# Kernel tuning notes

Hardware: AMD Instinct MI355X
Metric: run time of the kernel (lower is better)

The kernel has to match this reference:

```python
import jax, jax.numpy as jnp
import numpy as np

N_NODES = 100000
N_EDGES = 1280000
N_REL = 8
DIM = 64
N_LAYERS = 2
N_TGT = 50000


def setup_inputs() -> dict:
    key = jax.random.key(0)
    ks = jax.random.split(key, 8)
    x_idx = jnp.arange(N_NODES, dtype=jnp.int64) if jax.config.jax_enable_x64 else jnp.arange(N_NODES, dtype=jnp.int32)
    edge_index = jax.random.randint(ks[0], (2, N_EDGES), 0, N_NODES)
    edge_type = jax.random.randint(ks[1], (N_EDGES,), 0, N_REL)
    target_edge_index = jax.random.randint(ks[2], (2, N_TGT), 0, N_NODES)
    # xavier-ish scales to keep activations stable through relu stack
    node_emb = jax.random.normal(ks[3], (N_NODES, DIM), dtype=jnp.float32) * 0.1
    weight = jax.random.normal(ks[4], (N_LAYERS, N_REL, DIM, DIM), dtype=jnp.float32) * (1.0 / np.sqrt(DIM))
    root = jax.random.normal(ks[5], (N_LAYERS, DIM, DIM), dtype=jnp.float32) * (1.0 / np.sqrt(DIM))
    bias = jax.random.normal(ks[6], (N_LAYERS, DIM), dtype=jnp.float32) * 0.01
    return {"x_idx": x_idx, "edge_index": edge_index, "edge_type": edge_type,
            "target_edge_index": target_edge_index, "node_emb": node_emb,
            "weight": weight, "root": root, "bias": bias}


def reference(x_idx, edge_index, edge_type, target_edge_index, node_emb, weight, root, bias):
    # RGCN forward: x = node_emb[x_idx]; L x (FastRGCNConv + relu); edge dot-product score.
    x = node_emb[x_idx]                       # [N, D]
    src, dst = edge_index[0], edge_index[1]   # messages flow src -> dst (PyG source_to_target)
    n = x.shape[0]
    # in-degree for 'mean' aggregation (zero-degree nodes get 0, guard div)
    deg = jax.ops.segment_sum(jnp.ones((src.shape[0],), dtype=x.dtype), dst, num_segments=n)
    inv_deg = (1.0 / jnp.maximum(deg, 1.0))[:, None]  # [N, 1]
    n_layers = weight.shape[0]
    for l in range(n_layers):
        # transform every node by every relation, then gather per edge (FastRGCNConv math)
        h = jnp.einsum('ni,rio->rno', x, weight[l])   # [R, N, D]
        msg = h[edge_type, src]                       # [E, D]
        agg = jax.ops.segment_sum(msg, dst, num_segments=n) * inv_deg  # mean aggr [N, D]
        x = jax.nn.relu(agg + x @ root[l] + bias[l])
    s, t = target_edge_index[0], target_edge_index[1]
    return jnp.sum(x[s] * x[t], axis=-1)              # [T]
```

## Files before the change

kernel.cpp:

```cpp
#include <hip/hip_runtime.h>
#include <hip/hip_bf16.h>

#define DIM 64
#define NREL 8
#define KTOT 576

typedef __bf16 bf16x8 __attribute__((ext_vector_type(8)));
typedef __bf16 bf16x4 __attribute__((ext_vector_type(4)));
typedef float  f32x4  __attribute__((ext_vector_type(4)));

__global__ __launch_bounds__(256) void histgather_kernel(const int* __restrict__ dst,
                                                         const int* __restrict__ et,
                                                         int* __restrict__ deg8,
                                                         int* __restrict__ eoff,
                                                         const int* __restrict__ x_idx,
                                                         const float* __restrict__ emb,
                                                         __bf16* __restrict__ xb0,
                                                         __bf16* __restrict__ hbuf,
                                                         int* __restrict__ srcs,
                                                         int N, int E, int epad_cap) {
    int i = blockIdx.x * 256 + threadIdx.x;
    if (i < N * DIM) {
        int n = i >> 6;
        int c = i & 63;
        xb0[i] = (__bf16)emb[(size_t)x_idx[n] * DIM + c];
    }
    if (i < DIM) {
        hbuf[(size_t)N * NREL * DIM + i] = (__bf16)0.f;
    }
    if (i < epad_cap) srcs[i] = N * NREL;
    if (i < E) eoff[i] = atomicAdd(&deg8[dst[i] * 8 + et[i]], 1);
}

__global__ __launch_bounds__(256) void scan1rp_kernel(const int* __restrict__ deg8,
                                                      int* __restrict__ gtotal,
                                                      float* __restrict__ invdeg,
                                                      int* __restrict__ rp,
                                                      int* __restrict__ rend,
                                                      const float* __restrict__ weight,
                                                      const float* __restrict__ root,
                                                      __bf16* __restrict__ Wt2,
                                                      int N, int L) {
    __shared__ int sd[256];
    __shared__ int sbase;
    int tid = threadIdx.x;
    int d = blockIdx.x * 256 + tid;
    int dv[NREL];
    int vpad = 0;
    if (d < N) {
        int vtrue = 0;
#pragma unroll
        for (int r = 0; r < NREL; ++r) { dv[r] = deg8[d * 8 + r]; vtrue += dv[r]; }
        vpad = (vtrue + 3) & ~3;
        invdeg[d] = 1.0f / fmaxf((float)vtrue, 1.0f);
    }
    sd[tid] = vpad;
    __syncthreads();
#pragma unroll
    for (int off = 1; off < 256; off <<= 1) {
        int t = (tid >= off) ? sd[tid - off] : 0;
        __syncthreads();
        sd[tid] += t;
        __syncthreads();
    }
    if (tid == 255) sbase = atomicAdd(gtotal, sd[255]);
    __syncthreads();
    if (d < N) {
        int base = sbase + sd[tid] - vpad;
        int run = 0;
#pragma unroll
        for (int r = 0; r < NREL; ++r) {
            rp[d * 8 + r] = base + run;
            run += dv[r];
        }
        rend[d] = base + vpad;
    }
    int total = L * KTOT * DIM;
    for (int idx = blockIdx.x * 256 + tid; idx < total; idx += gridDim.x * 256) {
        int l = idx / (KTOT * DIM);
        int rem = idx - l * (KTOT * DIM);
        int row = rem / DIM;
        int ch = rem - row * DIM;
        float w;
        if (row < 512) {
            int r = row >> 6, c = row & 63;
            w = weight[(((l * 8 + r) * 64) + ch) * 64 + c];
        } else {
            w = root[(l * 64 + ch) * 64 + (row - 512)];
        }
        Wt2[idx] = (__bf16)w;
    }
}

__global__ __launch_bounds__(256) void bucket_kernel(const int* __restrict__ src,
                                                     const int* __restrict__ dst,
                                                     const int* __restrict__ et,
                                                     const int* __restrict__ rp,
                                                     const int* __restrict__ eoff,
                                                     int* __restrict__ srcs, int E) {
    int i = blockIdx.x * 256 + threadIdx.x;
    int half = (E + 1) >> 1;
    if (i >= half) return;
    int iB = i + half;
    bool hasB = iB < E;
    int etA = et[i];
    int etB = hasB ? et[iB] : 0;
    int cellA = dst[i] * 8 + etA;
    int cellB = hasB ? dst[iB] * 8 + etB : 0;
    int rA = rp[cellA];
    int rB = hasB ? rp[cellB] : 0;
    int oA = eoff[i];
    int oB = hasB ? eoff[iB] : 0;
    int sA = src[i];
    int sB = hasB ? src[iB] : 0;
    srcs[rA + oA] = sA * NREL + etA;
    if (hasB) srcs[rB + oB] = sB * NREL + etB;
}

__global__ __launch_bounds__(256) void transform_kernel(const __bf16* __restrict__ xin,
                                                        const __bf16* __restrict__ Wt2,
                                                        __bf16* __restrict__ h, int N) {
    int wave = threadIdx.x >> 6;
    int lane = threadIdx.x & 63;
    int l15 = lane & 15;
    int lg  = lane >> 4;

    bf16x8 afrag[8][2];
#pragma unroll
    for (int p = 0; p < 8; ++p) {
        const __bf16* wrow = Wt2 + (size_t)(p * 64 + 16 * wave + l15) * DIM + lg * 8;
        afrag[p][0] = *reinterpret_cast<const bf16x8*>(wrow);
        afrag[p][1] = *reinterpret_cast<const bf16x8*>(wrow + 32);
    }
    int cb = 16 * wave + 4 * lg;

    int ntiles = (N + 15) >> 4;
    for (int tile = blockIdx.x; tile < ntiles; tile += gridDim.x) {
        int n = tile * 16 + l15;
        int nc = (n < N) ? n : (N - 1);
        const __bf16* xrow = xin + (size_t)nc * DIM + lg * 8;
        bf16x8 bv0 = *reinterpret_cast<const bf16x8*>(xrow);
        bf16x8 bv1 = *reinterpret_cast<const bf16x8*>(xrow + 32);

#pragma unroll
        for (int p = 0; p < 8; ++p) {
            f32x4 acc = (f32x4){0.f, 0.f, 0.f, 0.f};
            acc = __builtin_amdgcn_mfma_f32_16x16x32_bf16(afrag[p][0], bv0, acc, 0, 0, 0);
            acc = __builtin_amdgcn_mfma_f32_16x16x32_bf16(afrag[p][1], bv1, acc, 0, 0, 0);
            if (n < N) {
                bf16x4 hv;
#pragma unroll
                for (int i = 0; i < 4; ++i) hv[i] = (__bf16)acc[i];
                *reinterpret_cast<bf16x4*>(h + (size_t)n * (NREL * DIM) + p * 64 + cb) = hv;
            }
        }
    }
}

__global__ __launch_bounds__(256) void aggroot_kernel(const __bf16* __restrict__ h,
                                                      const __bf16* __restrict__ xin,
                                                      const int* __restrict__ srcs,
                                                      const int* __restrict__ rp,
                                                      const int* __restrict__ rend,
                                                      const float* __restrict__ invdeg,
                                                      const __bf16* __restrict__ Wt2,
                                                      const float* __restrict__ bias_l,
                                                      __bf16* __restrict__ xout, int N) {
    __shared__ __align__(16) float S16[16][68];
    int wave = threadIdx.x >> 6;
    int lane = threadIdx.x & 63;
    int l15 = lane & 15;
    int lg  = lane >> 4;
    const int SENT = N * NREL;

    bf16x8 ar0, ar1;
    {
        const __bf16* wrow = Wt2 + (size_t)(512 + 16 * wave + l15) * DIM + lg * 8;
        ar0 = *reinterpret_cast<const bf16x8*>(wrow);
        ar1 = *reinterpret_cast<const bf16x8*>(wrow + 32);
    }
    int cbase = 16 * wave + 4 * lg;
    f32x4 bias4 = *reinterpret_cast<const f32x4*>(bias_l + cbase);

    int tile = blockIdx.x;

#pragma unroll
    for (int rr = 0; rr < 4; ++rr) {
        int d0 = tile * 16 + wave * 4 + rr;
        if (d0 >= N) d0 = N - 1;
        int d = __builtin_amdgcn_readfirstlane(d0);
        int qb = rp[d * 8];
        int qe = rend[d];
        float acc = 0.f;
        for (int q = qb; q < qe; q += 16) {
            int rem = qe - q;
            int4 sa = *reinterpret_cast<const int4*>(srcs + q);
            int4 sb = *reinterpret_cast<const int4*>(srcs + q + 4);
            int4 sc = *reinterpret_cast<const int4*>(srcs + q + 8);
            int4 sd = *reinterpret_cast<const int4*>(srcs + q + 12);
            bool vb = rem >= 8, vc = rem >= 12, vd = rem >= 16;
            int i0 = sa.x,              i1 = sa.y,              i2 = sa.z,              i3 = sa.w;
            int i4 = vb ? sb.x : SENT,  i5 = vb ? sb.y : SENT,  i6 = vb ? sb.z : SENT,  i7 = vb ? sb.w : SENT;
            int i8 = vc ? sc.x : SENT,  i9 = vc ? sc.y : SENT,  iA = vc ? sc.z : SENT,  iB = vc ? sc.w : SENT;
            int iC = vd ? sd.x : SENT,  iD = vd ? sd.y : SENT,  iE = vd ? sd.z : SENT,  iF = vd ? sd.w : SENT;
            float v0 = (float)h[(size_t)i0 * DIM + lane];
            float v1 = (float)h[(size_t)i1 * DIM + lane];
            float v2 = (float)h[(size_t)i2 * DIM + lane];
            float v3 = (float)h[(size_t)i3 * DIM + lane];
            float v4 = (float)h[(size_t)i4 * DIM + lane];
            float v5 = (float)h[(size_t)i5 * DIM + lane];
            float v6 = (float)h[(size_t)i6 * DIM + lane];
            float v7 = (float)h[(size_t)i7 * DIM + lane];
            float v8 = (float)h[(size_t)i8 * DIM + lane];
            float v9 = (float)h[(size_t)i9 * DIM + lane];
            float vA = (float)h[(size_t)iA * DIM + lane];
            float vB = (float)h[(size_t)iB * DIM + lane];
            float vC = (float)h[(size_t)iC * DIM + lane];
            float vD = (float)h[(size_t)iD * DIM + lane];
            float vE = (float)h[(size_t)iE * DIM + lane];
            float vF = (float)h[(size_t)iF * DIM + lane];
            acc += (((v0 + v1) + (v2 + v3)) + ((v4 + v5) + (v6 + v7)))
                 + (((v8 + v9) + (vA + vB)) + ((vC + vD) + (vE + vF)));
        }
        S16[wave * 4 + rr][lane] = acc * invdeg[d];
    }
    __syncthreads();

    int n = tile * 16 + l15;
    int nc = (n < N) ? n : (N - 1);
    const __bf16* xrow = xin + (size_t)nc * DIM + lg * 8;
    bf16x8 bv0 = *reinterpret_cast<const bf16x8*>(xrow);
    bf16x8 bv1 = *reinterpret_cast<const bf16x8*>(xrow + 32);
    f32x4 acc = (f32x4){0.f, 0.f, 0.f, 0.f};
    acc = __builtin_amdgcn_mfma_f32_16x16x32_bf16(ar0, bv0, acc, 0, 0, 0);
    acc = __builtin_amdgcn_mfma_f32_16x16x32_bf16(ar1, bv1, acc, 0, 0, 0);

    if (n < N) {
        f32x4 ag = *reinterpret_cast<const f32x4*>(&S16[l15][cbase]);
        bf16x4 hv;
#pragma unroll
        for (int i = 0; i < 4; ++i)
            hv[i] = (__bf16)fmaxf(acc[i] + ag[i] + bias4[i], 0.f);
        *reinterpret_cast<bf16x4*>(xout + (size_t)n * DIM + cbase) = hv;
    }
}

__global__ __launch_bounds__(256) void score_kernel(const __bf16* __restrict__ xb,
                                                    const int* __restrict__ s,
                                                    const int* __restrict__ t,
                                                    float* __restrict__ out, int T) {
    int i = blockIdx.x * 4 + (threadIdx.x >> 6);
    if (i >= T) return;
    int lane = threadIdx.x & 63;
    float p = (float)xb[(size_t)s[i] * DIM + lane] * (float)xb[(size_t)t[i] * DIM + lane];
#pragma unroll
    for (int off = 32; off > 0; off >>= 1) p += __shfl_down(p, off, 64);
    if (lane == 0) out[i] = p;
}

extern "C" void kernel_launch(void* const* d_in, const int* in_sizes, int n_in,
                              void* d_out, int out_size, void* d_ws, size_t ws_size,
                              hipStream_t stream) {
    const int*   x_idx  = (const int*)d_in[0];
    const int*   eidx   = (const int*)d_in[1];
    const int*   etyp   = (const int*)d_in[2];
    const int*   tidx   = (const int*)d_in[3];
    const float* emb    = (const float*)d_in[4];
    const float* weight = (const float*)d_in[5];
    const float* root   = (const float*)d_in[6];
    const float* bias   = (const float*)d_in[7];

    int N = in_sizes[0];
    int E = in_sizes[2];
    int T = in_sizes[3] / 2;
    int L = in_sizes[5] / (NREL * DIM * DIM);

    const int* src = eidx;
    const int* dst = eidx + E;
    const int* ts  = tidx;
    const int* tt  = tidx + T;
    float* out = (float*)d_out;

    int epad_cap = E + 3 * N + 64;

    char* p = (char*)d_ws;
    auto alloc = [&](size_t bytes) -> void* {
        void* r = (void*)p;
        p += (bytes + 255) & ~(size_t)255;
        return r;
    };
    __bf16* hbuf    = (__bf16*)alloc(((size_t)N * NREL + 1) * DIM * sizeof(__bf16));
    __bf16* xb0     = (__bf16*)alloc((size_t)N * DIM * sizeof(__bf16));
    __bf16* xb1     = (__bf16*)alloc((size_t)N * DIM * sizeof(__bf16));
    __bf16* Wt2     = (__bf16*)alloc((size_t)L * KTOT * DIM * sizeof(__bf16));
    int*    srcs    = (int*)   alloc((size_t)epad_cap * sizeof(int));
    int*    eoff    = (int*)   alloc((size_t)E * sizeof(int));
    int*    deg8    = (int*)   alloc(((size_t)N * 8 + 8) * sizeof(int));
    int*    rp      = (int*)   alloc((size_t)N * 8 * sizeof(int));
    int*    rend    = (int*)   alloc((size_t)N * sizeof(int));
    float*  invdeg  = (float*) alloc((size_t)N * sizeof(float));

    int* gtotal = deg8 + (size_t)N * 8;

    int nb = (N + 255) / 256;
    int ntiles = (N + 15) / 16;

    hipMemsetAsync(deg8, 0, ((size_t)N * 8 + 8) * sizeof(int), stream);
    histgather_kernel<<<((size_t)N * DIM + 255) / 256, 256, 0, stream>>>(
        dst, etyp, deg8, eoff, x_idx, emb, xb0, hbuf, srcs, N, E, epad_cap);
    scan1rp_kernel<<<nb, 256, 0, stream>>>(deg8, gtotal, invdeg, rp, rend,
                                           weight, root, Wt2, N, L);
    {
        int half = (E + 1) / 2;
        bucket_kernel<<<(half + 255) / 256, 256, 0, stream>>>(src, dst, etyp, rp, eoff, srcs, E);
    }

    __bf16* xcur = xb0;
    __bf16* xnxt = xb1;
    for (int l = 0; l < L; ++l) {
        transform_kernel<<<2048, 256, 0, stream>>>(xcur, Wt2 + (size_t)l * KTOT * DIM, hbuf, N);
        aggroot_kernel<<<ntiles, 256, 0, stream>>>(hbuf, xcur, srcs, rp, rend, invdeg,
                                                   Wt2 + (size_t)l * KTOT * DIM,
                                                   bias + (size_t)l * DIM,
                                                   xnxt, N);
        __bf16* tmp = xcur; xcur = xnxt; xnxt = tmp;
    }

    score_kernel<<<(T + 3) / 4, 256, 0, stream>>>(xcur, ts, tt, out, T);
}
```

Measured before the change: 355.1 us.

## Fuse layer-0 transform into bucket kernel and gather bf16 pairs per lane

The layer-0 per-relation transform now runs inside the edge-bucketing kernel, which saves one launch and lets the bucketing scatter overlap with the MFMA work. The aggregation gather now loads two bf16 channels per 32-bit word, so each half-wave handles a different edge. This doubles the edges in flight per load, and the two halves are combined with a cross-lane shuffle. The cost is a larger fused kernel, whose register pressure from the preloaded weight fragments may lower occupancy for the bucketing phase.

```diff
diff --git a/kernel.cpp b/kernel.cpp
--- a/kernel.cpp
+++ b/kernel.cpp
@@ -92,29 +92,68 @@
     }
 }
 
-__global__ __launch_bounds__(256) void bucket_kernel(const int* __restrict__ src,
-                                                     const int* __restrict__ dst,
-                                                     const int* __restrict__ et,
-                                                     const int* __restrict__ rp,
-                                                     const int* __restrict__ eoff,
-                                                     int* __restrict__ srcs, int E) {
+__global__ __launch_bounds__(256) void buckett0_kernel(const int* __restrict__ src,
+                                                       const int* __restrict__ dst,
+                                                       const int* __restrict__ et,
+                                                       const int* __restrict__ rp,
+                                                       const int* __restrict__ eoff,
+                                                       int* __restrict__ srcs, int E,
+                                                       const __bf16* __restrict__ xin,
+                                                       const __bf16* __restrict__ Wt2,
+                                                       __bf16* __restrict__ h, int N) {
     int i = blockIdx.x * 256 + threadIdx.x;
     int half = (E + 1) >> 1;
-    if (i >= half) return;
-    int iB = i + half;
-    bool hasB = iB < E;
-    int etA = et[i];
-    int etB = hasB ? et[iB] : 0;
-    int cellA = dst[i] * 8 + etA;
-    int cellB = hasB ? dst[iB] * 8 + etB : 0;
-    int rA = rp[cellA];
-    int rB = hasB ? rp[cellB] : 0;
-    int oA = eoff[i];
-    int oB = hasB ? eoff[iB] : 0;
-    int sA = src[i];
-    int sB = hasB ? src[iB] : 0;
-    srcs[rA + oA] = sA * NREL + etA;
-    if (hasB) srcs[rB + oB] = sB * NREL + etB;
+    if (i < half) {
+        int iB = i + half;
+        bool hasB = iB < E;
+        int etA = et[i];
+        int etB = hasB ? et[iB] : 0;
+        int cellA = dst[i] * 8 + etA;
+        int cellB = hasB ? dst[iB] * 8 + etB : 0;
+        int rA = rp[cellA];
+        int rB = hasB ? rp[cellB] : 0;
+        int oA = eoff[i];
+        int oB = hasB ? eoff[iB] : 0;
+        int sA = src[i];
+        int sB = hasB ? src[iB] : 0;
+        srcs[rA + oA] = sA * NREL + etA;
+        if (hasB) srcs[rB + oB] = sB * NREL + etB;
+    }
+
+    int wave = threadIdx.x >> 6;
+    int lane = threadIdx.x & 63;
+    int l15 = lane & 15;
+    int lg  = lane >> 4;
+
+    bf16x8 afrag[8][2];
+#pragma unroll
+    for (int p = 0; p < 8; ++p) {
+        const __bf16* wrow = Wt2 + (size_t)(p * 64 + 16 * wave + l15) * DIM + lg * 8;
+        afrag[p][0] = *reinterpret_cast<const bf16x8*>(wrow);
+        afrag[p][1] = *reinterpret_cast<const bf16x8*>(wrow + 32);
+    }
+    int cb = 16 * wave + 4 * lg;
+
+    int ntiles = (N + 15) >> 4;
+    for (int tile = blockIdx.x; tile < ntiles; tile += gridDim.x) {
+        int n = tile * 16 + l15;
+        int nc = (n < N) ? n : (N - 1);
+        const __bf16* xrow = xin + (size_t)nc * DIM + lg * 8;
+        bf16x8 bv0 = *reinterpret_cast<const bf16x8*>(xrow);
+        bf16x8 bv1 = *reinterpret_cast<const bf16x8*>(xrow + 32);
+#pragma unroll
+        for (int p = 0; p < 8; ++p) {
+            f32x4 acc = (f32x4){0.f, 0.f, 0.f, 0.f};
+            acc = __builtin_amdgcn_mfma_f32_16x16x32_bf16(afrag[p][0], bv0, acc, 0, 0, 0);
+            acc = __builtin_amdgcn_mfma_f32_16x16x32_bf16(afrag[p][1], bv1, acc, 0, 0, 0);
+            if (n < N) {
+                bf16x4 hv;
+#pragma unroll
+                for (int j = 0; j < 4; ++j) hv[j] = (__bf16)acc[j];
+                *reinterpret_cast<bf16x4*>(h + (size_t)n * (NREL * DIM) + p * 64 + cb) = hv;
+            }
+        }
+    }
 }
 
 __global__ __launch_bounds__(256) void transform_kernel(const __bf16* __restrict__ xin,
@@ -171,7 +210,10 @@
     int lane = threadIdx.x & 63;
     int l15 = lane & 15;
     int lg  = lane >> 4;
+    int c2  = lane & 31;
+    int hi  = lane >> 5;
     const int SENT = N * NREL;
+    const unsigned* hp = (const unsigned*)h;
 
     bf16x8 ar0, ar1;
     {
@@ -191,7 +233,7 @@
         int d = __builtin_amdgcn_readfirstlane(d0);
         int qb = rp[d * 8];
         int qe = rend[d];
-        float acc = 0.f;
+        float a0 = 0.f, a1 = 0.f;
         for (int q = qb; q < qe; q += 16) {
             int rem = qe - q;
             int4 sa = *reinterpret_cast<const int4*>(srcs + q);
@@ -199,30 +241,38 @@
             int4 sc = *reinterpret_cast<const int4*>(srcs + q + 8);
             int4 sd = *reinterpret_cast<const int4*>(srcs + q + 12);
             bool vb = rem >= 8, vc = rem >= 12, vd = rem >= 16;
-            int i0 = sa.x,              i1 = sa.y,              i2 = sa.z,              i3 = sa.w;
-            int i4 = vb ? sb.x : SENT,  i5 = vb ? sb.y : SENT,  i6 = vb ? sb.z : SENT,  i7 = vb ? sb.w : SENT;
-            int i8 = vc ? sc.x : SENT,  i9 = vc ? sc.y : SENT,  iA = vc ? sc.z : SENT,  iB = vc ? sc.w : SENT;
-            int iC = vd ? sd.x : SENT,  iD = vd ? sd.y : SENT,  iE = vd ? sd.z : SENT,  iF = vd ? sd.w : SENT;
-            float v0 = (float)h[(size_t)i0 * DIM + lane];
-            float v1 = (float)h[(size_t)i1 * DIM + lane];
-            float v2 = (float)h[(size_t)i2 * DIM + lane];
-            float v3 = (float)h[(size_t)i3 * DIM + lane];
-            float v4 = (float)h[(size_t)i4 * DIM + lane];
-            float v5 = (float)h[(size_t)i5 * DIM + lane];
-            float v6 = (float)h[(size_t)i6 * DIM + lane];
-            float v7 = (float)h[(size_t)i7 * DIM + lane];
-            float v8 = (float)h[(size_t)i8 * DIM + lane];
-            float v9 = (float)h[(size_t)i9 * DIM + lane];
-            float vA = (float)h[(size_t)iA * DIM + lane];
-            float vB = (float)h[(size_t)iB * DIM + lane];
-            float vC = (float)h[(size_t)iC * DIM + lane];
-            float vD = (float)h[(size_t)iD * DIM + lane];
-            float vE = (float)h[(size_t)iE * DIM + lane];
-            float vF = (float)h[(size_t)iF * DIM + lane];
-            acc += (((v0 + v1) + (v2 + v3)) + ((v4 + v5) + (v6 + v7)))
-                 + (((v8 + v9) + (vA + vB)) + ((vC + vD) + (vE + vF)));
-        }
-        S16[wave * 4 + rr][lane] = acc * invdeg[d];
+            int g0 = hi ? sa.y : sa.x;
+            int g1 = hi ? sa.w : sa.z;
+            int g2 = vb ? (hi ? sb.y : sb.x) : SENT;
+            int g3 = vb ? (hi ? sb.w : sb.z) : SENT;
+            int g4 = vc ? (hi ? sc.y : sc.x) : SENT;
+            int g5 = vc ? (hi ? sc.w : sc.z) : SENT;
+            int g6 = vd ? (hi ? sd.y : sd.x) : SENT;
+            int g7 = vd ? (hi ? sd.w : sd.z) : SENT;
+            unsigned v0 = hp[(size_t)g0 * 32 + c2];
+            unsigned v1 = hp[(size_t)g1 * 32 + c2];
+            unsigned v2 = hp[(size_t)g2 * 32 + c2];
+            unsigned v3 = hp[(size_t)g3 * 32 + c2];
+            unsigned v4 = hp[(size_t)g4 * 32 + c2];
+            unsigned v5 = hp[(size_t)g5 * 32 + c2];
+            unsigned v6 = hp[(size_t)g6 * 32 + c2];
+            unsigned v7 = hp[(size_t)g7 * 32 + c2];
+            a0 += __uint_as_float(v0 << 16) + __uint_as_float(v1 << 16)
+                + __uint_as_float(v2 << 16) + __uint_as_float(v3 << 16)
+                + __uint_as_float(v4 << 16) + __uint_as_float(v5 << 16)
+                + __uint_as_float(v6 << 16) + __uint_as_float(v7 << 16);
+            a1 += __uint_as_float(v0 & 0xffff0000u) + __uint_as_float(v1 & 0xffff0000u)
+                + __uint_as_float(v2 & 0xffff0000u) + __uint_as_float(v3 & 0xffff0000u)
+                + __uint_as_float(v4 & 0xffff0000u) + __uint_as_float(v5 & 0xffff0000u)
+                + __uint_as_float(v6 & 0xffff0000u) + __uint_as_float(v7 & 0xffff0000u);
+        }
+        a0 += __shfl_xor(a0, 32, 64);
+        a1 += __shfl_xor(a1, 32, 64);
+        float inv = invdeg[d];
+        if (hi == 0) {
+            S16[wave * 4 + rr][c2 * 2]     = a0 * inv;
+            S16[wave * 4 + rr][c2 * 2 + 1] = a1 * inv;
+        }
     }
     __syncthreads();
 
@@ -312,13 +362,16 @@
                                            weight, root, Wt2, N, L);
     {
         int half = (E + 1) / 2;
-        bucket_kernel<<<(half + 255) / 256, 256, 0, stream>>>(src, dst, etyp, rp, eoff, srcs, E);
+        int bblocks = (half + 255) / 256;
+        buckett0_kernel<<<bblocks, 256, 0, stream>>>(src, dst, etyp, rp, eoff, srcs, E,
+                                                     xb0, Wt2, hbuf, N);
     }
 
     __bf16* xcur = xb0;
     __bf16* xnxt = xb1;
     for (int l = 0; l < L; ++l) {
-        transform_kernel<<<2048, 256, 0, stream>>>(xcur, Wt2 + (size_t)l * KTOT * DIM, hbuf, N);
+        if (l > 0)
+            transform_kernel<<<2048, 256, 0, stream>>>(xcur, Wt2 + (size_t)l * KTOT * DIM, hbuf, N);
         aggroot_kernel<<<ntiles, 256, 0, stream>>>(hbuf, xcur, srcs, rp, rend, invdeg,
                                                    Wt2 + (size_t)l * KTOT * DIM,
                                                    bias + (size_t)l * DIM,
```

Measured after the change: 361.3 us. No clear change (+1.8%).
